# Performance work log

Measured on AMD Instinct MI355X. Metric: run time of the kernel, lower is better.

## Reference

```python
import jax, jax.numpy as jnp
import numpy as np

EMBED_DIM = 1024
NUM_HEADS = 16
HEAD_DIM = EMBED_DIM // NUM_HEADS
WINDOW = 3
N_RAND = 3
BLOCK = 64
BATCH = 2
SEQ = 2048


def _bigbird_mask(seq_len: int) -> np.ndarray:
    """Global + sliding-window + random block mask. True = attend.
    Deterministic (fixed numpy seed) stand-in for np.random.choice in the
    original; the mask is data-independent so it is a compile-time constant."""
    nb = -(-seq_len // BLOCK)  # ceil division
    mask = np.zeros((seq_len, seq_len), dtype=bool)
    g = min(BLOCK, seq_len)
    mask[:g, :] = True  # global rows
    mask[:, :g] = True  # global cols
    blk = np.arange(seq_len) // BLOCK
    # sliding window: block distance <= WINDOW (matches start/end block loop)
    mask |= np.abs(blk[:, None] - blk[None, :]) <= WINDOW
    rng = np.random.RandomState(0)
    for b in range(1, nb):
        avail = [x for x in range(1, nb) if abs(x - b) > WINDOW]
        if avail:
            sel = rng.choice(avail, size=min(N_RAND, len(avail)), replace=False)
            s0, s1 = b * BLOCK, min(seq_len, (b + 1) * BLOCK)
            for rb in sel:
                mask[s0:s1, rb * BLOCK:min(seq_len, (rb + 1) * BLOCK)] = True
    return mask


def setup_inputs() -> dict:
    key = jax.random.key(0)
    ks = jax.random.split(key, 9)
    E = EMBED_DIM
    std = E ** -0.5
    return {
        "hidden_states": jax.random.normal(ks[0], (BATCH, SEQ, E), jnp.float32),
        "wq": jax.random.normal(ks[1], (E, E), jnp.float32) * std,
        "bq": jnp.zeros((E,), jnp.float32),
        "wk": jax.random.normal(ks[2], (E, E), jnp.float32) * std,
        "bk": jnp.zeros((E,), jnp.float32),
        "wv": jax.random.normal(ks[3], (E, E), jnp.float32) * std,
        "bv": jnp.zeros((E,), jnp.float32),
        "wo": jax.random.normal(ks[4], (E, E), jnp.float32) * std,
        "bo": jnp.zeros((E,), jnp.float32),
    }


def reference(hidden_states, wq, bq, wk, bk, wv, bv, wo, bo):
    B, S, E = hidden_states.shape
    D = HEAD_DIM
    scale = D ** -0.5

    def proj(w, b):  # (B,S,E) -> (B,H,S,D)
        return (hidden_states @ w.T + b).reshape(B, S, NUM_HEADS, D).transpose(0, 2, 1, 3)

    q = proj(wq, bq)
    k = proj(wk, bk)
    v = proj(wv, bv)
    scores = jnp.einsum('bhqd,bhkd->bhqk', q, k) * scale  # dense, masked post-hoc (as in source)
    mask = jnp.asarray(_bigbird_mask(S))
    scores = jnp.where(mask[None, None, :, :], scores, -jnp.inf)
    attn = jax.nn.softmax(scores, axis=-1)
    out = jnp.einsum('bhqk,bhkd->bhqd', attn, v)
    out = out.transpose(0, 2, 1, 3).reshape(B, S, E)
    return out @ wo.T + bo
```

## Files before the change

kernel.cpp:

```cpp
#include <hip/hip_runtime.h>
#include <cstdint>
#include <math.h>


#define DEVI __device__ __forceinline__

typedef __bf16 bf16x8 __attribute__((ext_vector_type(8)));
typedef float floatx4 __attribute__((ext_vector_type(4)));
typedef unsigned short u16x8 __attribute__((ext_vector_type(8)));
typedef unsigned short u16x4 __attribute__((ext_vector_type(4)));
typedef unsigned short ushort_t;

typedef const __attribute__((address_space(1))) void* gptr_as1;
typedef __attribute__((address_space(3))) void* lptr_as3;

DEVI ushort_t f2bf(float f) {
  unsigned u = __float_as_uint(f);
  unsigned r = ((u >> 16) & 1u) + 0x7fffu;
  return (ushort_t)((u + r) >> 16);
}

DEVI void lds_load16(void* lds, const void* g) {
  __builtin_amdgcn_global_load_lds((gptr_as1)g, (lptr_as3)lds, 16, 0, 0);
}

DEVI floatx4 mfma16(bf16x8 a, bf16x8 b, floatx4 c) {
  return __builtin_amdgcn_mfma_f32_16x16x32_bf16(a, b, c, 0, 0, 0);
}

#define BARR() do { asm volatile("" ::: "memory"); \
                    __builtin_amdgcn_s_barrier();  \
                    asm volatile("" ::: "memory"); } while (0)
#define LGKM0() asm volatile("s_waitcnt lgkmcnt(0)" ::: "memory")
#define VMC(N) asm volatile("s_waitcnt vmcnt(" #N ")" ::: "memory")

struct MTState { unsigned mt[624]; int mti; };

constexpr unsigned mt_next(MTState& s) {
  if (s.mti >= 624) {
    for (int k = 0; k < 624; ++k) {
      unsigned y = (s.mt[k] & 0x80000000u) | (s.mt[(k + 1) % 624] & 0x7fffffffu);
      unsigned v = s.mt[(k + 397) % 624] ^ (y >> 1);
      if (y & 1u) v ^= 0x9908b0dfu;
      s.mt[k] = v;
    }
    s.mti = 0;
  }
  unsigned y = s.mt[s.mti++];
  y ^= y >> 11;
  y ^= (y << 7) & 0x9d2c5680u;
  y ^= (y << 15) & 0xefc60000u;
  y ^= y >> 18;
  return y;
}

constexpr unsigned mt_interval(MTState& s, unsigned mx) {
  if (mx == 0u) return 0u;
  unsigned msk = mx;
  msk |= msk >> 1; msk |= msk >> 2; msk |= msk >> 4; msk |= msk >> 8; msk |= msk >> 16;
  unsigned v = mt_next(s) & msk;
  while (v > mx) v = mt_next(s) & msk;
  return v;
}

struct MaskPack { unsigned char list[32][32]; int cnt[32]; };

constexpr MaskPack make_pack() {
  unsigned char m[32][32] = {};
  for (int i = 0; i < 32; ++i)
    for (int j = 0; j < 32; ++j) {
      int d = i - j; if (d < 0) d = -d;
      m[i][j] = (i == 0 || j == 0 || d <= 3) ? (unsigned char)1 : (unsigned char)0;
    }
  MTState st{};
  st.mt[0] = 0u;
  for (int i = 1; i < 624; ++i)
    st.mt[i] = 1812433253u * (st.mt[i - 1] ^ (st.mt[i - 1] >> 30)) + (unsigned)i;
  st.mti = 624;
  for (int b = 1; b < 32; ++b) {
    int avail[32] = {}; int n = 0;
    for (int x = 1; x < 32; ++x) {
      int d = x - b; if (d < 0) d = -d;
      if (d > 3) avail[n++] = x;
    }
    if (n == 0) continue;
    int perm[32] = {};
    for (int i = 0; i < n; ++i) perm[i] = i;
    for (int i = n - 1; i > 0; --i) {
      unsigned j = mt_interval(st, (unsigned)i);
      int t = perm[i]; perm[i] = perm[(int)j]; perm[(int)j] = t;
    }
    int take = n < 3 ? n : 3;
    for (int s = 0; s < take; ++s) m[b][avail[perm[s]]] = 1;
  }
  MaskPack P{};
  for (int i = 0; i < 32; ++i) {
    int c = 0;
    for (int j = 0; j < 32; ++j)
      if (m[i][j]) P.list[i][c++] = (unsigned char)j;
    P.cnt[i] = c;
  }
  return P;
}

__constant__ MaskPack MP = make_pack();

__global__ __launch_bounds__(256) void cvt_all(
    const float* __restrict__ hs, const float* __restrict__ wq,
    const float* __restrict__ wk, const float* __restrict__ wv,
    const float* __restrict__ wo,
    ushort_t* __restrict__ hs_bf, ushort_t* __restrict__ wq_bf,
    ushort_t* __restrict__ wk_bf, ushort_t* __restrict__ wv_bf,
    ushort_t* __restrict__ wo_bf) {
  const int i = blockIdx.x * 256 + threadIdx.x;
  const float* s;
  ushort_t* d;
  int j;
  if (i < 1048576) {
    s = hs; d = hs_bf; j = i;
  } else {
    const int t = (i - 1048576) >> 18;
    j = (i - 1048576) & 262143;
    s = t == 0 ? wq : (t == 1 ? wk : (t == 2 ? wv : wo));
    d = t == 0 ? wq_bf : (t == 1 ? wk_bf : (t == 2 ? wv_bf : wo_bf));
  }
  const float4 f = ((const float4*)s)[j];
  u16x4 o;
  o.x = f2bf(f.x); o.y = f2bf(f.y); o.z = f2bf(f.z); o.w = f2bf(f.w);
  ((u16x4*)d)[j] = o;
}

DEVI void stage_half(ushort_t* ldsb, const ushort_t* g, int w, int l) {
  lds_load16(ldsb + w * 1024 + l * 8, g);
  lds_load16(ldsb + w * 1024 + 512 + l * 8, g + 8192);
}

DEVI void rdA(bf16x8 (&a)[4][2], const ushort_t* base, int wm, int li, int quad) {
#pragma unroll
  for (int mi = 0; mi < 4; ++mi) {
    const int rh = wm * 64 + mi * 16 + li;
    const int sw = rh & 7;
#pragma unroll
    for (int ks = 0; ks < 2; ++ks)
      a[mi][ks] = *(const bf16x8*)(base + rh * 64 + (((ks * 4 + quad) ^ sw) << 3));
  }
}

DEVI void rdB(bf16x8 (&b)[2][2], const ushort_t* base, int wn, int li, int quad) {
#pragma unroll
  for (int ni = 0; ni < 2; ++ni) {
    const int rh = wn * 32 + ni * 16 + li;
    const int sw = rh & 7;
#pragma unroll
    for (int ks = 0; ks < 2; ++ks)
      b[ni][ks] = *(const bf16x8*)(base + rh * 64 + (((ks * 4 + quad) ^ sw) << 3));
  }
}

DEVI void mm16(floatx4 (&c)[4][2], const bf16x8 (&a)[4][2], const bf16x8 (&b)[2][2]) {
  __builtin_amdgcn_s_setprio(1);
#pragma unroll
  for (int ks = 0; ks < 2; ++ks)
#pragma unroll
    for (int mi = 0; mi < 4; ++mi)
#pragma unroll
      for (int ni = 0; ni < 2; ++ni)
        c[mi][ni] = mfma16(a[mi][ks], b[ni][ks], c[mi][ni]);
  __builtin_amdgcn_s_setprio(0);
}

__global__ __launch_bounds__(512, 2) void gemm_qkv_fused(
    const ushort_t* __restrict__ A,
    const ushort_t* __restrict__ W0, const ushort_t* __restrict__ W1,
    const ushort_t* __restrict__ W2,
    const float* __restrict__ bq, const float* __restrict__ bk,
    const float* __restrict__ bv,
    ushort_t* __restrict__ Qo, ushort_t* __restrict__ Ko,
    ushort_t* __restrict__ Vt) {
  __shared__ alignas(16) ushort_t LDS[2][2][2][8192];
  const int tid = threadIdx.x;
  const int w = tid >> 6, l = tid & 63, quad = l >> 4, li = l & 15;
  const int wm = w >> 2, wn = w & 3;
  const int bid = blockIdx.x;
  const int swz = (bid & 7) * 24 + (bid >> 3);
  const int m0 = (swz / 12) << 8;
  const int n0g = (swz % 12) << 8;
  const int z = n0g >> 10, n0l = n0g & 1023;
  const ushort_t* Bw = z == 0 ? W0 : (z == 1 ? W1 : W2);
  const float* bias = z == 0 ? bq : (z == 1 ? bk : bv);

  const int rst = w * 16 + (l >> 3);
  const int cst = ((l & 7) ^ (l >> 3)) << 3;
  const ushort_t* gA = A + (size_t)(m0 + rst) * 1024 + cst;
  const ushort_t* gB = Bw + (size_t)(n0l + rst) * 1024 + cst;

  const floatx4 fz = {0.0f, 0.0f, 0.0f, 0.0f};
  floatx4 acc[2][2][4][2];
#pragma unroll
  for (int qm = 0; qm < 2; ++qm)
#pragma unroll
    for (int qn = 0; qn < 2; ++qn)
#pragma unroll
      for (int mi = 0; mi < 4; ++mi)
#pragma unroll
        for (int ni = 0; ni < 2; ++ni) acc[qm][qn][mi][ni] = fz;

  bf16x8 a[4][2], b0[2][2], b1[2][2];

  stage_half(&LDS[0][0][0][0], gA, w, l);
  stage_half(&LDS[0][0][1][0], gA + 131072, w, l);
  stage_half(&LDS[0][1][0][0], gB, w, l);
  stage_half(&LDS[0][1][1][0], gB + 131072, w, l);
  stage_half(&LDS[1][0][0][0], gA + 64, w, l);
  stage_half(&LDS[1][1][0][0], gB + 64, w, l);
  stage_half(&LDS[1][1][1][0], gB + 131072 + 64, w, l);
  VMC(6);
  BARR();

#pragma unroll 1
  for (int it = 0; it < 8; ++it) {
    const bool pf = (it < 7);
    const int o_cy = (2 * it + 1) * 64;
    const int o_x = (2 * it + 2) * 64;
    const int o_y = (2 * it + 3) * 64;

    rdA(a, &LDS[0][0][0][0], wm, li, quad);
    rdB(b0, &LDS[0][1][0][0], wn, li, quad);
    stage_half(&LDS[1][0][1][0], gA + 131072 + o_cy, w, l);
    BARR(); LGKM0();
    mm16(acc[0][0], a, b0);
    BARR();

    rdB(b1, &LDS[0][1][1][0], wn, li, quad);
    if (pf) stage_half(&LDS[0][0][0][0], gA + o_x, w, l);
    BARR(); LGKM0();
    mm16(acc[0][1], a, b1);
    BARR();

    rdA(a, &LDS[0][0][1][0], wm, li, quad);
    if (pf) stage_half(&LDS[0][1][0][0], gB + o_x, w, l);
    BARR(); LGKM0();
    mm16(acc[1][0], a, b0);
    BARR();

    if (pf) stage_half(&LDS[0][1][1][0], gB + 131072 + o_x, w, l);
    BARR(); LGKM0();
    mm16(acc[1][1], a, b1);
    if (pf) { VMC(6); } else { VMC(0); }
    BARR();

    rdA(a, &LDS[1][0][0][0], wm, li, quad);
    rdB(b0, &LDS[1][1][0][0], wn, li, quad);
    if (pf) stage_half(&LDS[0][0][1][0], gA + 131072 + o_x, w, l);
    BARR(); LGKM0();
    mm16(acc[0][0], a, b0);
    BARR();

    rdB(b1, &LDS[1][1][1][0], wn, li, quad);
    if (pf) stage_half(&LDS[1][0][0][0], gA + o_y, w, l);
    BARR(); LGKM0();
    mm16(acc[0][1], a, b1);
    BARR();

    rdA(a, &LDS[1][0][1][0], wm, li, quad);
    if (pf) stage_half(&LDS[1][1][0][0], gB + o_y, w, l);
    BARR(); LGKM0();
    mm16(acc[1][0], a, b0);
    BARR();

    if (pf) stage_half(&LDS[1][1][1][0], gB + 131072 + o_y, w, l);
    BARR(); LGKM0();
    mm16(acc[1][1], a, b1);
    if (pf) { VMC(6); }
    BARR();
  }

#pragma unroll
  for (int Qm = 0; Qm < 2; ++Qm)
#pragma unroll
    for (int Qn = 0; Qn < 2; ++Qn)
#pragma unroll
      for (int ni = 0; ni < 2; ++ni) {
        const int col = n0l + Qn * 128 + wn * 32 + ni * 16 + li;
        const float bb_ = bias[col];
        if (z == 2) {
          const int hh = col >> 6, dd = col & 63;
#pragma unroll
          for (int mi = 0; mi < 4; ++mi) {
            const int row0 = m0 + Qm * 128 + wm * 64 + mi * 16 + quad * 4;
            const int bb = row0 >> 11, s0 = row0 & 2047;
            u16x4 pk;
#pragma unroll
            for (int r = 0; r < 4; ++r) pk[r] = f2bf(acc[Qm][Qn][mi][ni][r] + bb_);
            *(u16x4*)(Vt + (size_t)((bb * 16 + hh) * 64 + dd) * 2048 + s0) = pk;
          }
        } else {
          ushort_t* Co = (z == 0) ? Qo : Ko;
#pragma unroll
          for (int mi = 0; mi < 4; ++mi)
#pragma unroll
            for (int r = 0; r < 4; ++r) {
              const int row = m0 + Qm * 128 + wm * 64 + mi * 16 + quad * 4 + r;
              Co[(size_t)row * 1024 + col] = f2bf(acc[Qm][Qn][mi][ni][r] + bb_);
            }
        }
      }
}

__global__ __launch_bounds__(256) void gemm_o64(
    const ushort_t* __restrict__ A, const ushort_t* __restrict__ W,
    const float* __restrict__ bias, float* __restrict__ C) {
  constexpr int N = 1024, K = 1024;
  __shared__ alignas(16) ushort_t As[64 * 32];
  __shared__ alignas(16) ushort_t Bs[128 * 32];
  const int tid = threadIdx.x;
  const int w = tid >> 6, l = tid & 63, quad = l >> 4, li = l & 15;
  const int m0 = blockIdx.x * 64, n0 = blockIdx.y * 128;
  const int wm = (w >> 1) * 32, wn = (w & 1) * 64;

  const int lofA = w * 512 + l * 8;
  const int rA = lofA >> 5, cA = lofA & 31;
  const int lofB0 = (w * 2 + 0) * 512 + l * 8;
  const int lofB1 = (w * 2 + 1) * 512 + l * 8;
  const int rB0 = lofB0 >> 5, cB0 = lofB0 & 31;
  const int rB1 = lofB1 >> 5, cB1 = lofB1 & 31;
  const ushort_t* gA = A + (size_t)(m0 + rA) * K + cA;
  const ushort_t* gB0 = W + (size_t)(n0 + rB0) * K + cB0;
  const ushort_t* gB1 = W + (size_t)(n0 + rB1) * K + cB1;

  const floatx4 fzero = {0.0f, 0.0f, 0.0f, 0.0f};
  floatx4 acc[2][4];
#pragma unroll
  for (int i = 0; i < 2; ++i)
#pragma unroll
    for (int j = 0; j < 4; ++j) acc[i][j] = fzero;

  for (int k0 = 0; k0 < K; k0 += 32) {
    lds_load16(As + lofA, gA + k0);
    lds_load16(Bs + lofB0, gB0 + k0);
    lds_load16(Bs + lofB1, gB1 + k0);
    __syncthreads();
    bf16x8 af[2], bfr[4];
#pragma unroll
    for (int mi = 0; mi < 2; ++mi)
      af[mi] = *(const bf16x8*)(As + (wm + mi * 16 + li) * 32 + quad * 8);
#pragma unroll
    for (int ni = 0; ni < 4; ++ni)
      bfr[ni] = *(const bf16x8*)(Bs + (wn + ni * 16 + li) * 32 + quad * 8);
#pragma unroll
    for (int mi = 0; mi < 2; ++mi)
#pragma unroll
      for (int ni = 0; ni < 4; ++ni)
        acc[mi][ni] = mfma16(af[mi], bfr[ni], acc[mi][ni]);
    __syncthreads();
  }

#pragma unroll
  for (int ni = 0; ni < 4; ++ni) {
    const int col = n0 + wn + ni * 16 + li;
    const float bv = bias[col];
#pragma unroll
    for (int mi = 0; mi < 2; ++mi) {
#pragma unroll
      for (int r = 0; r < 4; ++r) {
        const int row = m0 + wm + mi * 16 + quad * 4 + r;
        C[(size_t)row * N + col] = acc[mi][ni][r] + bv;
      }
    }
  }
}

__global__ __launch_bounds__(256) void attn_kernel(
    const ushort_t* __restrict__ Q, const ushort_t* __restrict__ Kg,
    const ushort_t* __restrict__ Vtg, ushort_t* __restrict__ O,
    float* __restrict__ OP, float* __restrict__ LP) {
  __shared__ alignas(16) ushort_t Kls[64 * 72];
  __shared__ alignas(16) ushort_t Vls[64 * 72];
  __shared__ alignas(16) ushort_t Ps[4][16 * 72];

  const int tid = threadIdx.x;
  const int w = tid >> 6, l = tid & 63, quad = l >> 4, li = l & 15;
  const int hb = blockIdx.x;
  const int y = blockIdx.y;
  const bool partial = (y >= 31);
  const int qb = partial ? 0 : (y + 1);
  const int p = partial ? (y - 31) : 0;
  const int base = p * 11;
  const int nact = partial ? (32 - base < 11 ? 32 - base : 11) : MP.cnt[qb];

  const int h = hb & 15, b = hb >> 4;
  const size_t qoff = (size_t)b * 2048 * 1024 + (size_t)h * 64;
  const size_t vtoff = (size_t)hb * 64 * 2048;

  const int qrow = qb * 64 + w * 16 + li;
  bf16x8 aq0 = *(const bf16x8*)(Q + qoff + (size_t)qrow * 1024 + quad * 8);
  bf16x8 aq1 = *(const bf16x8*)(Q + qoff + (size_t)qrow * 1024 + 32 + quad * 8);
#pragma unroll
  for (int j = 0; j < 8; ++j) {
    aq0[j] = (__bf16)((float)aq0[j] * 0.125f);
    aq1[j] = (__bf16)((float)aq1[j] * 0.125f);
  }

  const floatx4 fzero = {0.0f, 0.0f, 0.0f, 0.0f};
  floatx4 o_acc[4];
  float lp[4];
#pragma unroll
  for (int nt = 0; nt < 4; ++nt) o_acc[nt] = fzero;
#pragma unroll
  for (int r = 0; r < 4; ++r) lp[r] = 0.0f;

  const int r0 = w * 16 + (l >> 3);
  const int r1 = r0 + 8;
  const int cb = (l & 7) * 8;
  const ushort_t* kg0 = Kg + qoff + (size_t)r0 * 1024 + cb;
  const ushort_t* kg1 = Kg + qoff + (size_t)r1 * 1024 + cb;
  const ushort_t* vg0 = Vtg + vtoff + (size_t)r0 * 2048 + cb;
  const ushort_t* vg1 = Vtg + vtoff + (size_t)r1 * 2048 + cb;
  ushort_t* kd0 = Kls + r0 * 72 + cb;
  ushort_t* kd1 = Kls + r1 * 72 + cb;
  ushort_t* vd0 = Vls + r0 * 72 + cb;
  ushort_t* vd1 = Vls + r1 * 72 + cb;
  ushort_t* PsW = Ps[w];

  int kb = MP.list[qb][base];
  {
    const u16x8 a0 = *(const u16x8*)(kg0 + (size_t)kb * 65536);
    const u16x8 a1 = *(const u16x8*)(kg1 + (size_t)kb * 65536);
    const u16x8 b0 = *(const u16x8*)(vg0 + kb * 64);
    const u16x8 b1 = *(const u16x8*)(vg1 + kb * 64);
    *(u16x8*)kd0 = a0; *(u16x8*)kd1 = a1;
    *(u16x8*)vd0 = b0; *(u16x8*)vd1 = b1;
  }

  for (int i = 0; i < nact; ++i) {
    const int kbn = (i + 1 < nact) ? (int)MP.list[qb][base + i + 1] : 0;
    __syncthreads();

    floatx4 s[4];
#pragma unroll
    for (int nt = 0; nt < 4; ++nt) {
      const bf16x8 bk0 = *(const bf16x8*)(Kls + (nt * 16 + li) * 72 + quad * 8);
      const bf16x8 bk1 = *(const bf16x8*)(Kls + (nt * 16 + li) * 72 + 32 + quad * 8);
      s[nt] = mfma16(aq1, bk1, mfma16(aq0, bk0, fzero));
    }

#pragma unroll
    for (int nt = 0; nt < 4; ++nt)
#pragma unroll
      for (int r = 0; r < 4; ++r) {
        const float e = __expf(s[nt][r]);
        lp[r] += e;
        PsW[(quad * 4 + r) * 72 + nt * 16 + li] = f2bf(e);
      }

#pragma unroll
    for (int c = 0; c < 2; ++c) {
      const bf16x8 pa = *(const bf16x8*)(PsW + li * 72 + c * 32 + quad * 8);
#pragma unroll
      for (int nt = 0; nt < 4; ++nt) {
        const bf16x8 vb = *(const bf16x8*)(Vls + (nt * 16 + li) * 72 + c * 32 + quad * 8);
        o_acc[nt] = mfma16(pa, vb, o_acc[nt]);
      }
    }

    __syncthreads();
    if (i + 1 < nact) {
      const u16x8 a0 = *(const u16x8*)(kg0 + (size_t)kbn * 65536);
      const u16x8 a1 = *(const u16x8*)(kg1 + (size_t)kbn * 65536);
      const u16x8 b0 = *(const u16x8*)(vg0 + kbn * 64);
      const u16x8 b1 = *(const u16x8*)(vg1 + kbn * 64);
      *(u16x8*)kd0 = a0; *(u16x8*)kd1 = a1;
      *(u16x8*)vd0 = b0; *(u16x8*)vd1 = b1;
    }
  }

#pragma unroll
  for (int stp = 1; stp <= 8; stp <<= 1)
#pragma unroll
    for (int r = 0; r < 4; ++r) lp[r] += __shfl_xor(lp[r], stp);

  if (!partial) {
#pragma unroll
    for (int r = 0; r < 4; ++r) {
      const float rinv = 1.0f / lp[r];
#pragma unroll
      for (int nt = 0; nt < 4; ++nt) {
        const float ov = o_acc[nt][r] * rinv;
        O[qoff + (size_t)(qb * 64 + w * 16 + quad * 4 + r) * 1024 + nt * 16 + li] = f2bf(ov);
      }
    }
  } else {
    float* O32 = OP + (size_t)(hb * 3 + p) * 4096;
    float* LPp = LP + (hb * 3 + p) * 64;
#pragma unroll
    for (int r = 0; r < 4; ++r) {
      const int row = w * 16 + quad * 4 + r;
#pragma unroll
      for (int nt = 0; nt < 4; ++nt)
        O32[row * 64 + nt * 16 + li] = o_acc[nt][r];
      if (li == 0) LPp[row] = lp[r];
    }
  }
}

__global__ __launch_bounds__(256) void combine_qb0(
    const float* __restrict__ OP, const float* __restrict__ LP,
    ushort_t* __restrict__ O) {
  const int hb = blockIdx.x;
  const int b = hb >> 4, h = hb & 15;
  const float* o0 = OP + (size_t)hb * 3 * 4096;
  const float* l0 = LP + hb * 3 * 64;
  for (int idx = threadIdx.x; idx < 4096; idx += 256) {
    const int q = idx >> 6, d = idx & 63;
    const float s = o0[idx] + o0[4096 + idx] + o0[8192 + idx];
    const float lsum = l0[q] + l0[64 + q] + l0[128 + q];
    O[(size_t)b * 2048 * 1024 + (size_t)q * 1024 + h * 64 + d] = f2bf(s / lsum);
  }
}

extern "C" void kernel_launch(void* const* d_in, const int* in_sizes, int n_in,
                              void* d_out, int out_size, void* d_ws, size_t ws_size,
                              hipStream_t stream) {
  const float* hs = (const float*)d_in[0];
  const float* wq = (const float*)d_in[1];
  const float* bq = (const float*)d_in[2];
  const float* wk = (const float*)d_in[3];
  const float* bk = (const float*)d_in[4];
  const float* wv = (const float*)d_in[5];
  const float* bv = (const float*)d_in[6];
  const float* wo = (const float*)d_in[7];
  const float* bo = (const float*)d_in[8];
  float* out = (float*)d_out;

  char* ws = (char*)d_ws;
  ushort_t* hs_bf = (ushort_t*)(ws);
  ushort_t* wq_bf = (ushort_t*)(ws + (8ull << 20));
  ushort_t* wk_bf = (ushort_t*)(ws + (10ull << 20));
  ushort_t* wv_bf = (ushort_t*)(ws + (12ull << 20));
  ushort_t* wo_bf = (ushort_t*)(ws + (14ull << 20));
  ushort_t* Qb = (ushort_t*)(ws + (16ull << 20));
  ushort_t* Kb = (ushort_t*)(ws + (24ull << 20));
  ushort_t* Vt = (ushort_t*)(ws + (32ull << 20));
  ushort_t* AO = hs_bf;
  float* OP = (float*)(ws + (10ull << 20));
  float* LP = (float*)(ws + (10ull << 20) + (2ull << 20));
  LP = (float*)((char*)OP + 32 * 3 * 4096 * sizeof(float));

  cvt_all<<<8192, 256, 0, stream>>>(hs, wq, wk, wv, wo,
                                    hs_bf, wq_bf, wk_bf, wv_bf, wo_bf);

  gemm_qkv_fused<<<192, 512, 0, stream>>>(hs_bf, wq_bf, wk_bf, wv_bf,
                                          bq, bk, bv, Qb, Kb, Vt);

  dim3 ga(32, 34, 1);
  attn_kernel<<<ga, 256, 0, stream>>>(Qb, Kb, Vt, AO, OP, LP);

  combine_qb0<<<32, 256, 0, stream>>>(OP, LP, AO);

  dim3 go(64, 8, 1);
  gemm_o64<<<go, 256, 0, stream>>>(AO, wo_bf, bo, out);
}
```

Baseline: 183.0 us.

## Load K/V MFMA fragments directly from global memory, dropping shared-memory staging

The attention kernel no longer stages K and V tiles in LDS with block-wide barriers. Each wave now loads its MFMA operand fragments for K and V^T straight from global memory every iteration, and the loop is marked unroll 1. This removes the two __syncthreads per key block and frees LDS, and launch bounds now request 4 blocks per CU for higher occupancy. The cost is that all four waves redundantly fetch the same K/V data through the cache, the loads are less coalesced, and without the old prefetch overlap the kernel may stall on global-load latency.

Measured after the change: 248.1 us. 35.6% more time.

```diff
diff --git a/kernel.cpp b/kernel.cpp
--- a/kernel.cpp
+++ b/kernel.cpp
@@ -370,12 +370,10 @@
   }
 }
 
-__global__ __launch_bounds__(256) void attn_kernel(
+__global__ __launch_bounds__(256, 4) void attn_kernel(
     const ushort_t* __restrict__ Q, const ushort_t* __restrict__ Kg,
     const ushort_t* __restrict__ Vtg, ushort_t* __restrict__ O,
     float* __restrict__ OP, float* __restrict__ LP) {
-  __shared__ alignas(16) ushort_t Kls[64 * 72];
-  __shared__ alignas(16) ushort_t Vls[64 * 72];
   __shared__ alignas(16) ushort_t Ps[4][16 * 72];
 
   const int tid = threadIdx.x;
@@ -409,39 +407,33 @@
 #pragma unroll
   for (int r = 0; r < 4; ++r) lp[r] = 0.0f;
 
-  const int r0 = w * 16 + (l >> 3);
-  const int r1 = r0 + 8;
-  const int cb = (l & 7) * 8;
-  const ushort_t* kg0 = Kg + qoff + (size_t)r0 * 1024 + cb;
-  const ushort_t* kg1 = Kg + qoff + (size_t)r1 * 1024 + cb;
-  const ushort_t* vg0 = Vtg + vtoff + (size_t)r0 * 2048 + cb;
-  const ushort_t* vg1 = Vtg + vtoff + (size_t)r1 * 2048 + cb;
-  ushort_t* kd0 = Kls + r0 * 72 + cb;
-  ushort_t* kd1 = Kls + r1 * 72 + cb;
-  ushort_t* vd0 = Vls + r0 * 72 + cb;
-  ushort_t* vd1 = Vls + r1 * 72 + cb;
+  const ushort_t* kgb = Kg + qoff + (size_t)li * 1024 + quad * 8;
+  const ushort_t* vgb = Vtg + vtoff + (size_t)li * 2048 + quad * 8;
   ushort_t* PsW = Ps[w];
 
-  int kb = MP.list[qb][base];
-  {
-    const u16x8 a0 = *(const u16x8*)(kg0 + (size_t)kb * 65536);
-    const u16x8 a1 = *(const u16x8*)(kg1 + (size_t)kb * 65536);
-    const u16x8 b0 = *(const u16x8*)(vg0 + kb * 64);
-    const u16x8 b1 = *(const u16x8*)(vg1 + kb * 64);
-    *(u16x8*)kd0 = a0; *(u16x8*)kd1 = a1;
-    *(u16x8*)vd0 = b0; *(u16x8*)vd1 = b1;
-  }
-
+#pragma unroll 1
   for (int i = 0; i < nact; ++i) {
-    const int kbn = (i + 1 < nact) ? (int)MP.list[qb][base + i + 1] : 0;
-    __syncthreads();
+    const int kb = (int)MP.list[qb][base + i];
+    const ushort_t* kgp = kgb + (size_t)kb * 65536;
+    const ushort_t* vgp = vgb + kb * 64;
+
+    bf16x8 bk0[4], bk1[4];
+#pragma unroll
+    for (int nt = 0; nt < 4; ++nt) {
+      bk0[nt] = *(const bf16x8*)(kgp + nt * 16384);
+      bk1[nt] = *(const bf16x8*)(kgp + nt * 16384 + 32);
+    }
 
     floatx4 s[4];
 #pragma unroll
+    for (int nt = 0; nt < 4; ++nt)
+      s[nt] = mfma16(aq1, bk1[nt], mfma16(aq0, bk0[nt], fzero));
+
+    bf16x8 vb0[4], vb1[4];
+#pragma unroll
     for (int nt = 0; nt < 4; ++nt) {
-      const bf16x8 bk0 = *(const bf16x8*)(Kls + (nt * 16 + li) * 72 + quad * 8);
-      const bf16x8 bk1 = *(const bf16x8*)(Kls + (nt * 16 + li) * 72 + 32 + quad * 8);
-      s[nt] = mfma16(aq1, bk1, mfma16(aq0, bk0, fzero));
+      vb0[nt] = *(const bf16x8*)(vgp + nt * 32768);
+      vb1[nt] = *(const bf16x8*)(vgp + nt * 32768 + 32);
     }
 
 #pragma unroll
@@ -457,20 +449,8 @@
     for (int c = 0; c < 2; ++c) {
       const bf16x8 pa = *(const bf16x8*)(PsW + li * 72 + c * 32 + quad * 8);
 #pragma unroll
-      for (int nt = 0; nt < 4; ++nt) {
-        const bf16x8 vb = *(const bf16x8*)(Vls + (nt * 16 + li) * 72 + c * 32 + quad * 8);
-        o_acc[nt] = mfma16(pa, vb, o_acc[nt]);
-      }
-    }
-
-    __syncthreads();
-    if (i + 1 < nact) {
-      const u16x8 a0 = *(const u16x8*)(kg0 + (size_t)kbn * 65536);
-      const u16x8 a1 = *(const u16x8*)(kg1 + (size_t)kbn * 65536);
-      const u16x8 b0 = *(const u16x8*)(vg0 + kbn * 64);
-      const u16x8 b1 = *(const u16x8*)(vg1 + kbn * 64);
-      *(u16x8*)kd0 = a0; *(u16x8*)kd1 = a1;
-      *(u16x8*)vd0 = b0; *(u16x8*)vd1 = b1;
+      for (int nt = 0; nt < 4; ++nt)
+        o_acc[nt] = mfma16(pa, c ? vb1[nt] : vb0[nt], o_acc[nt]);
     }
   }
 
@@ -543,8 +523,7 @@
   ushort_t* Vt = (ushort_t*)(ws + (32ull << 20));
   ushort_t* AO = hs_bf;
   float* OP = (float*)(ws + (10ull << 20));
-  float* LP = (float*)(ws + (10ull << 20) + (2ull << 20));
-  LP = (float*)((char*)OP + 32 * 3 * 4096 * sizeof(float));
+  float* LP = (float*)((char*)OP + 32 * 3 * 4096 * sizeof(float));
 
   cvt_all<<<8192, 256, 0, stream>>>(hs, wq, wk, wv, wo,
                                     hs_bf, wq_bf, wk_bf, wv_bf, wo_bf);
```
